# Performance work log

Hardware: AMD Instinct MI355X
Metric: run time of the kernel (lower is better)

## Reference

```python
import jax, jax.numpy as jnp
import numpy as np

OFFSET_FP32 = np.uint32(1064828928)  # L-mul exponent-bias correction constant for float32


def lmul_matmul(A, B):
    """Approximate A @ B (m,n)x(n,p) via integer-add-as-multiply on float bit patterns.

    Torch ref adds bit patterns in int64 then truncates with .to(torch.uint32),
    i.e. arithmetic mod 2**32 -- identical to plain uint32 wraparound addition,
    so we stay in uint32 and avoid needing x64 mode.
    """
    Au = jax.lax.bitcast_convert_type(A, jnp.uint32)          # (m, n)
    Bu = jax.lax.bitcast_convert_type(B, jnp.uint32)          # (n, p)
    prod_bits = Au[:, :, None] + Bu[None, :, :] - OFFSET_FP32  # (m, n, p), wraps mod 2^32
    prod = jax.lax.bitcast_convert_type(prod_bits, jnp.float32)
    return prod.sum(axis=1)                                    # (m, p)


def setup_inputs() -> dict:
    key = jax.random.key(0)
    k1, k2, k3 = jax.random.split(key, 3)
    m, n, p = 256, 512, 512
    x = jax.random.normal(k1, (m, n), dtype=jnp.float32)
    bound = 1.0 / np.sqrt(n)  # kaiming_uniform(a=sqrt(5)) -> U(-1/sqrt(fan_in), 1/sqrt(fan_in))
    weight = jax.random.uniform(k2, (p, n), dtype=jnp.float32, minval=-bound, maxval=bound)
    bias = jax.random.uniform(k3, (p,), dtype=jnp.float32, minval=-bound, maxval=bound)
    return {"x": x, "weight": weight, "bias": bias}


def reference(x, weight, bias):
    out = lmul_matmul(x, weight.T)
    return out + bias
```

## Files before the change

kernel.cpp:

```cpp
#include <hip/hip_runtime.h>
#include <stdint.h>


#define OFFSET_FP32 1064828928u

constexpr int M = 256;
constexpr int N = 512;
constexpr int P = 512;

constexpr int BP = 64;
constexpr int BM = 8;
constexpr int TM = 2;
constexpr int KC = 128;
constexpr int NC = N / KC;

__global__ __launch_bounds__(256) void lmul_linear_kernel(
    const uint32_t* __restrict__ xb,
    const uint32_t* __restrict__ wb,
    const float*    __restrict__ bias,
    float*          __restrict__ out)
{
    __shared__ uint32_t Bs[NC][BP][KC];

    const int tid     = threadIdx.x;
    const int p_local = tid & (BP - 1);
    const int wq      = __builtin_amdgcn_readfirstlane(tid >> 6);

    const int p0 = blockIdx.y * BP;
    const int m0 = blockIdx.x * BM + wq * TM;

    const int lane  = tid & 63;
    const int gran  = lane & 31;
    const int rhalf = lane >> 5;

    auto stage = [&](int c) {
        #pragma unroll
        for (int i = 0; i < 8; ++i) {
            const int row = wq * 16 + i * 2 + rhalf;
            const uint32_t* src = wb + (size_t)(p0 + row) * N + c * KC
                                     + ((gran ^ (row & 7)) * 4);
            uint32_t* dst = &Bs[c][wq * 16 + i * 2][0];
            __builtin_amdgcn_global_load_lds(
                (const __attribute__((address_space(1))) uint32_t*)src,
                (__attribute__((address_space(3))) uint32_t*)dst,
                16, 0, 0);
        }
    };

    float acc[TM][4] = {};
    const int rot = p_local & 7;

    stage(0);
    __syncthreads();

    #pragma unroll
    for (int c = 0; c < NC; ++c) {
        if (c + 1 < NC) stage(c + 1);

        const uint32_t* brow = &Bs[c][p_local][0];
        const uint32_t* xr0  = xb + (size_t)(m0 + 0) * N + c * KC;
        const uint32_t* xr1  = xb + (size_t)(m0 + 1) * N + c * KC;

        #pragma unroll 8
        for (int j = 0; j < KC / 4; ++j) {
            const uint4 b  = *(const uint4*)&brow[(j ^ rot) * 4];
            const uint4 a0 = *(const uint4*)(xr0 + j * 4);
            const uint4 a1 = *(const uint4*)(xr1 + j * 4);
            acc[0][0] += __uint_as_float((a0.x - OFFSET_FP32) + b.x);
            acc[0][1] += __uint_as_float((a0.y - OFFSET_FP32) + b.y);
            acc[0][2] += __uint_as_float((a0.z - OFFSET_FP32) + b.z);
            acc[0][3] += __uint_as_float((a0.w - OFFSET_FP32) + b.w);
            acc[1][0] += __uint_as_float((a1.x - OFFSET_FP32) + b.x);
            acc[1][1] += __uint_as_float((a1.y - OFFSET_FP32) + b.y);
            acc[1][2] += __uint_as_float((a1.z - OFFSET_FP32) + b.z);
            acc[1][3] += __uint_as_float((a1.w - OFFSET_FP32) + b.w);
        }

        if (c + 1 < NC) __syncthreads();
    }

    const int   p  = p0 + p_local;
    const float bv = bias[p];
    #pragma unroll
    for (int r = 0; r < TM; ++r) {
        out[(size_t)(m0 + r) * P + p] =
            (acc[r][0] + acc[r][1]) + (acc[r][2] + acc[r][3]) + bv;
    }
}

extern "C" void kernel_launch(void* const* d_in, const int* in_sizes, int n_in,
                              void* d_out, int out_size, void* d_ws, size_t ws_size,
                              hipStream_t stream) {
    const uint32_t* xb   = (const uint32_t*)d_in[0];
    const uint32_t* wb   = (const uint32_t*)d_in[1];
    const float*    bias = (const float*)d_in[2];
    float*          out  = (float*)d_out;

    dim3 grid(M / BM, P / BP);
    dim3 block(256);
    lmul_linear_kernel<<<grid, block, 0, stream>>>(xb, wb, bias, out);
}
```

Before: 67.85 us.

## Split K across waves with LDS reduction and 512-thread blocks

Each block now runs 8 waves: 4 K-slices by 2 row groups, and each thread covers 4 rows instead of 2. W is staged in two halves instead of four chunks, and the per-K-slice partial sums are reduced through shared memory before bias is added. The aim is to raise in-block parallelism and x reuse per B load and to shorten each wave's serial accumulation chain. The cost is an extra reduction pass with another barrier, plus more registers and LDS per block, which may lower occupancy.

Result: faster. 64.13 us (-5.5%).

```diff
diff --git a/kernel.cpp b/kernel.cpp
--- a/kernel.cpp
+++ b/kernel.cpp
@@ -8,38 +8,35 @@
 constexpr int N = 512;
 constexpr int P = 512;
 
+constexpr int BM = 8;
 constexpr int BP = 64;
-constexpr int BM = 8;
-constexpr int TM = 2;
-constexpr int KC = 128;
-constexpr int NC = N / KC;
+constexpr int TM = 4;
 
-__global__ __launch_bounds__(256) void lmul_linear_kernel(
+__global__ __launch_bounds__(512) void lmul_linear_kernel(
     const uint32_t* __restrict__ xb,
     const uint32_t* __restrict__ wb,
     const float*    __restrict__ bias,
     float*          __restrict__ out)
 {
-    __shared__ uint32_t Bs[NC][BP][KC];
+    __shared__ uint32_t Bs[BP][N];
+    __shared__ float    Red[4][BM][BP];
 
-    const int tid     = threadIdx.x;
-    const int p_local = tid & (BP - 1);
-    const int wq      = __builtin_amdgcn_readfirstlane(tid >> 6);
+    const int tid  = threadIdx.x;
+    const int lane = tid & 63;
+    const int wq   = __builtin_amdgcn_readfirstlane(tid >> 6);
+    const int ks   = wq & 3;
+    const int mq   = wq >> 2;
 
     const int p0 = blockIdx.y * BP;
-    const int m0 = blockIdx.x * BM + wq * TM;
+    const int m0 = blockIdx.x * BM + mq * TM;
 
-    const int lane  = tid & 63;
-    const int gran  = lane & 31;
-    const int rhalf = lane >> 5;
-
-    auto stage = [&](int c) {
+    auto stage = [&](int h) {
         #pragma unroll
         for (int i = 0; i < 8; ++i) {
-            const int row = wq * 16 + i * 2 + rhalf;
-            const uint32_t* src = wb + (size_t)(p0 + row) * N + c * KC
-                                     + ((gran ^ (row & 7)) * 4);
-            uint32_t* dst = &Bs[c][wq * 16 + i * 2][0];
+            const int row = wq * 8 + i;
+            const uint32_t* src = wb + (size_t)(p0 + row) * N
+                                + (size_t)(h * 64 + (lane ^ (row & 7))) * 4;
+            uint32_t* dst = &Bs[row][h * 256];
             __builtin_amdgcn_global_load_lds(
                 (const __attribute__((address_space(1))) uint32_t*)src,
                 (__attribute__((address_space(3))) uint32_t*)dst,
@@ -48,24 +45,23 @@
     };
 
     float acc[TM][4] = {};
-    const int rot = p_local & 7;
+    const int rot = lane & 7;
 
-    stage(0);
-    __syncthreads();
+    const uint32_t* xr0 = xb + (size_t)(m0 + 0) * N;
+    const uint32_t* xr1 = xb + (size_t)(m0 + 1) * N;
+    const uint32_t* xr2 = xb + (size_t)(m0 + 2) * N;
+    const uint32_t* xr3 = xb + (size_t)(m0 + 3) * N;
 
-    #pragma unroll
-    for (int c = 0; c < NC; ++c) {
-        if (c + 1 < NC) stage(c + 1);
-
-        const uint32_t* brow = &Bs[c][p_local][0];
-        const uint32_t* xr0  = xb + (size_t)(m0 + 0) * N + c * KC;
-        const uint32_t* xr1  = xb + (size_t)(m0 + 1) * N + c * KC;
-
+    auto compute = [&](int h) {
+        const uint32_t* brow = &Bs[lane][(h * 64 + ks * 16) * 4];
+        const int xoff = h * 256 + ks * 64;
         #pragma unroll 8
-        for (int j = 0; j < KC / 4; ++j) {
+        for (int j = 0; j < 16; ++j) {
             const uint4 b  = *(const uint4*)&brow[(j ^ rot) * 4];
-            const uint4 a0 = *(const uint4*)(xr0 + j * 4);
-            const uint4 a1 = *(const uint4*)(xr1 + j * 4);
+            const uint4 a0 = *(const uint4*)(xr0 + xoff + j * 4);
+            const uint4 a1 = *(const uint4*)(xr1 + xoff + j * 4);
+            const uint4 a2 = *(const uint4*)(xr2 + xoff + j * 4);
+            const uint4 a3 = *(const uint4*)(xr3 + xoff + j * 4);
             acc[0][0] += __uint_as_float((a0.x - OFFSET_FP32) + b.x);
             acc[0][1] += __uint_as_float((a0.y - OFFSET_FP32) + b.y);
             acc[0][2] += __uint_as_float((a0.z - OFFSET_FP32) + b.z);
@@ -74,18 +70,35 @@
             acc[1][1] += __uint_as_float((a1.y - OFFSET_FP32) + b.y);
             acc[1][2] += __uint_as_float((a1.z - OFFSET_FP32) + b.z);
             acc[1][3] += __uint_as_float((a1.w - OFFSET_FP32) + b.w);
+            acc[2][0] += __uint_as_float((a2.x - OFFSET_FP32) + b.x);
+            acc[2][1] += __uint_as_float((a2.y - OFFSET_FP32) + b.y);
+            acc[2][2] += __uint_as_float((a2.z - OFFSET_FP32) + b.z);
+            acc[2][3] += __uint_as_float((a2.w - OFFSET_FP32) + b.w);
+            acc[3][0] += __uint_as_float((a3.x - OFFSET_FP32) + b.x);
+            acc[3][1] += __uint_as_float((a3.y - OFFSET_FP32) + b.y);
+            acc[3][2] += __uint_as_float((a3.z - OFFSET_FP32) + b.z);
+            acc[3][3] += __uint_as_float((a3.w - OFFSET_FP32) + b.w);
         }
+    };
 
-        if (c + 1 < NC) __syncthreads();
-    }
+    stage(0);
+    __syncthreads();
+    stage(1);
+    compute(0);
+    __syncthreads();
+    compute(1);
 
-    const int   p  = p0 + p_local;
-    const float bv = bias[p];
     #pragma unroll
-    for (int r = 0; r < TM; ++r) {
-        out[(size_t)(m0 + r) * P + p] =
-            (acc[r][0] + acc[r][1]) + (acc[r][2] + acc[r][3]) + bv;
-    }
+    for (int r = 0; r < TM; ++r)
+        Red[ks][mq * TM + r][lane] =
+            (acc[r][0] + acc[r][1]) + (acc[r][2] + acc[r][3]);
+    __syncthreads();
+
+    const int rr = tid >> 6;
+    const int p  = p0 + lane;
+    const float s = (Red[0][rr][lane] + Red[1][rr][lane])
+                  + (Red[2][rr][lane] + Red[3][rr][lane]);
+    out[(size_t)(blockIdx.x * BM + rr) * P + p] = s + bias[p];
 }
 
 extern "C" void kernel_launch(void* const* d_in, const int* in_sizes, int n_in,
@@ -97,6 +110,6 @@
     float*          out  = (float*)d_out;
 
     dim3 grid(M / BM, P / BP);
-    dim3 block(256);
+    dim3 block(512);
     lmul_linear_kernel<<<grid, block, 0, stream>>>(xb, wb, bias, out);
 }
```
